# Kernel tuning notes

Hardware: AMD Instinct MI355X
Metric: run time of the kernel (lower is better)

The kernel has to match this reference:

```python
import jax, jax.numpy as jnp
import numpy as np

N_NODES = 100000
N_EDGES = 3200000
N_FEAT = 128
N_CLASS = 40
K_HOPS = 2


def setup_inputs() -> dict:
    key = jax.random.key(0)
    k1, k2, k3 = jax.random.split(key, 3)
    feature = jax.random.normal(k1, (N_NODES, N_FEAT), dtype=jnp.float32)
    # Glorot-ish linear params (SGConv.lin)
    weight = jax.random.normal(k2, (N_CLASS, N_FEAT), dtype=jnp.float32) * (1.0 / np.sqrt(N_FEAT))
    bias = jnp.zeros((N_CLASS,), dtype=jnp.float32)
    edge_index = jax.random.randint(k3, (2, N_EDGES), 0, N_NODES, dtype=jnp.int64)
    return {"feature": feature, "weight": weight, "bias": bias,
            "edge_index": edge_index, "use_feature": 1}


def reference(feature, weight, bias, edge_index, use_feature):
    # use_feature is a Python int flag; SGC uses feature when true (identity otherwise)
    x = feature if use_feature else jnp.eye(feature.shape[0], feature.shape[1], dtype=feature.dtype)
    N = x.shape[0]

    # gcn_norm: add self-loops, symmetric normalization D^-1/2 (A+I) D^-1/2
    loops = jnp.arange(N, dtype=edge_index.dtype)
    row = jnp.concatenate([edge_index[0], loops])  # source nodes
    col = jnp.concatenate([edge_index[1], loops])  # target nodes
    ew = jnp.ones(row.shape[0], dtype=x.dtype)
    deg = jax.ops.segment_sum(ew, col, num_segments=N)  # in-degree incl. self-loop
    deg_inv_sqrt = jnp.where(deg > 0, jax.lax.rsqrt(jnp.maximum(deg, 1e-12)), 0.0)
    norm = deg_inv_sqrt[row] * deg_inv_sqrt[col]  # [E+N]

    # K-hop propagation: out[col] += norm * x[row]
    for _ in range(K_HOPS):
        x = jax.ops.segment_sum(norm[:, None] * x[row], col, num_segments=N)

    logits = x @ weight.T + bias  # [N, C]
    return jax.nn.log_softmax(logits, axis=1)
```

## Files before the change

### kernel.cpp

```cpp
#include <hip/hip_runtime.h>
#include <hip/hip_bf16.h>
#include <hip/hip_fp16.h>
#include <math.h>


#define N_NODES 100000
#define N_FEAT  128
#define N_CLASS 40

#define RANGE   256
#define NBALLOC 512
#define NBUSED  391
#define CAP     8704
#define P3BLK   6250
#define HALF_SPLIT 50000

typedef __attribute__((ext_vector_type(8))) short short8;
typedef __attribute__((ext_vector_type(4))) float floatx4;

__device__ __forceinline__ int edge_word(const int* ei, int elem, int is64) {
    return is64 ? ei[2 * elem] : ei[elem];
}

__global__ __launch_bounds__(256) void p3a_scatter(
    const int* __restrict__ ei, int E,
    int* __restrict__ bucketCount, unsigned int* __restrict__ tmp)
{
    __shared__ unsigned int srt[P3BLK];
    __shared__ unsigned short fb[P3BLK];
    __shared__ int hist[NBALLOC];
    __shared__ int lbase[NBALLOC];
    __shared__ int gbase[NBALLOC];
    __shared__ int cur[NBALLOC];
    __shared__ int sc[256];
    __shared__ int s_is64;
    int t = threadIdx.x;
    for (int i = t; i < NBALLOC; i += 256) hist[i] = 0;
    if (t < 64) {
        int nz = (ei[2 * t + 1] != 0) ? 1 : 0;
        unsigned long long bl = __ballot(nz);
        if (t == 0) s_is64 = (bl == 0ull) ? 1 : 0;
    }
    __syncthreads();
    int is64 = s_is64;
    int per = (E + gridDim.x - 1) / gridDim.x;
    int e0 = blockIdx.x * per;
    int e1 = min(E, e0 + per);
    int n = e1 - e0;
    for (int e = e0 + t; e < e1; e += 256) {
        int c = edge_word(ei, E + e, is64);
        atomicAdd(&hist[c >> 8], 1);
    }
    __syncthreads();
    int h0 = hist[2 * t], h1 = hist[2 * t + 1];
    sc[t] = h0 + h1;
    __syncthreads();
    for (int o = 1; o < 256; o <<= 1) {
        int y = (t >= o) ? sc[t - o] : 0;
        __syncthreads();
        sc[t] += y;
        __syncthreads();
    }
    int excl = sc[t] - (h0 + h1);
    lbase[2 * t] = excl;
    lbase[2 * t + 1] = excl + h0;
    cur[2 * t] = excl;
    cur[2 * t + 1] = excl + h0;
    gbase[2 * t]     = h0 ? atomicAdd(&bucketCount[2 * t], h0) : 0;
    gbase[2 * t + 1] = h1 ? atomicAdd(&bucketCount[2 * t + 1], h1) : 0;
    __syncthreads();
    for (int e = e0 + t; e < e1; e += 256) {
        int c = edge_word(ei, E + e, is64);
        int r = edge_word(ei, e, is64);
        int f = c >> 8;
        int p = atomicAdd(&cur[f], 1);
        srt[p] = ((unsigned)(c & 255) << 24) | (unsigned)r;
        fb[p] = (unsigned short)f;
    }
    __syncthreads();
    for (int i = t; i < n; i += 256) {
        int f = fb[i];
        int p = gbase[f] + (i - lbase[f]);
        if (p < CAP) tmp[(size_t)f * CAP + p] = srt[i];
    }
}

__global__ __launch_bounds__(256) void p4_sort(
    const unsigned int* __restrict__ tmp, const int* __restrict__ bucketCount,
    int* __restrict__ starts, int* __restrict__ mid, float* __restrict__ dis,
    int* __restrict__ srcsB, int N, int E)
{
    __shared__ int srt[CAP];
    __shared__ int hist[512];
    __shared__ int sc[256];
    __shared__ int cur[512];
    __shared__ int cnt[NBALLOC];
    __shared__ int base_s;
    int b = blockIdx.x, t = threadIdx.x;
    int g0 = b * RANGE;
    int gcnt = N - g0;
    if (gcnt > RANGE) gcnt = RANGE;
    for (int i = t; i < NBALLOC; i += 256) cnt[i] = bucketCount[i];
    __syncthreads();
    int p0 = cnt[2 * t], p1 = cnt[2 * t + 1];
    sc[t] = p0 + p1;
    __syncthreads();
    for (int o = 1; o < 256; o <<= 1) {
        int y = (t >= o) ? sc[t - o] : 0;
        __syncthreads();
        sc[t] += y;
        __syncthreads();
    }
    if (t == 0) {
        int pairs = b >> 1;
        int base = (pairs > 0) ? sc[pairs - 1] : 0;
        if (b & 1) base += cnt[b - 1];
        base_s = base;
        if (b == 0) starts[N_NODES] = E;
    }
    __syncthreads();
    int base = base_s;
    int n = cnt[b];
    int nr = min(n, CAP);
    const unsigned int* rec = tmp + (size_t)b * CAP;
    hist[t] = 0;
    hist[t + 256] = 0;
    __syncthreads();
    for (int i = t; i < nr; i += 256) {
        unsigned v = rec[i];
        int key = (int)((v >> 24) << 1) | (((v & 0xFFFFFFu) >= HALF_SPLIT) ? 1 : 0);
        atomicAdd(&hist[key], 1);
    }
    __syncthreads();
    int c0 = hist[2 * t], c1 = hist[2 * t + 1];
    sc[t] = c0 + c1;
    __syncthreads();
    for (int o = 1; o < 256; o <<= 1) {
        int y = (t >= o) ? sc[t - o] : 0;
        __syncthreads();
        sc[t] += y;
        __syncthreads();
    }
    int excl = sc[t] - (c0 + c1);
    if (t < gcnt) {
        starts[g0 + t] = base + excl;
        mid[g0 + t] = base + excl + c0;
        dis[g0 + t] = rsqrtf((float)(c0 + c1 + 1));
    }
    cur[2 * t] = excl;
    cur[2 * t + 1] = excl + c0;
    __syncthreads();
    for (int i = t; i < nr; i += 256) {
        unsigned v = rec[i];
        int src = (int)(v & 0xFFFFFFu);
        int key = (int)((v >> 24) << 1) | ((src >= HALF_SPLIT) ? 1 : 0);
        int p = atomicAdd(&cur[key], 1);
        srt[p] = src * 80;
    }
    __syncthreads();
    for (int i = t; i < nr; i += 256) srcsB[base + i] = srt[i];
}

__device__ __forceinline__ unsigned short f2bf(float f) {
    unsigned u = __float_as_uint(f);
    unsigned r = u + 0x7FFFu + ((u >> 16) & 1u);
    return (unsigned short)(r >> 16);
}
__device__ __forceinline__ __half2 u2h(unsigned w) {
    union { unsigned u; __half2 h; } c; c.u = w; return c.h;
}
__device__ __forceinline__ unsigned h2u(__half2 h) {
    union { unsigned u; __half2 h; } c; c.h = h; return c.u;
}

__global__ __launch_bounds__(256) void transform_mfma(
    const float* __restrict__ x, const float* __restrict__ W,
    const float* __restrict__ dis, unsigned short* __restrict__ t0, int N)
{
    __shared__ uint4 Wl[3 * 4 * 64];
    int t = threadIdx.x;
    for (int i = t; i < 3 * 4 * 64; i += 256) {
        int lane = i & 63;
        int kc = (i >> 6) & 3;
        int nt = i >> 8;
        int n = nt * 16 + (lane & 15);
        int k = kc * 32 + (lane >> 4) * 8;
        union { unsigned short s[8]; uint4 v; } u;
        #pragma unroll
        for (int j = 0; j < 8; ++j)
            u.s[j] = (n < N_CLASS) ? f2bf(W[n * N_FEAT + k + j]) : (unsigned short)0;
        Wl[i] = u.v;
    }
    __syncthreads();
    int wave = (blockIdx.x * blockDim.x + threadIdx.x) >> 6;
    int lane = threadIdx.x & 63;
    int ntile = (N + 15) / 16;
    if (wave >= ntile) return;
    int m = lane & 15, quad = lane >> 4;
    int row = wave * 16 + m;
    const short8* Wf = reinterpret_cast<const short8*>(Wl);
    floatx4 acc0 = {0.f, 0.f, 0.f, 0.f}, acc1 = acc0, acc2 = acc0;
    #pragma unroll
    for (int kc = 0; kc < 4; ++kc) {
        const float4* xr = reinterpret_cast<const float4*>(
            x + (size_t)row * N_FEAT + kc * 32 + quad * 8);
        float4 a0 = xr[0], a1 = xr[1];
        short8 af;
        af[0] = f2bf(a0.x); af[1] = f2bf(a0.y); af[2] = f2bf(a0.z); af[3] = f2bf(a0.w);
        af[4] = f2bf(a1.x); af[5] = f2bf(a1.y); af[6] = f2bf(a1.z); af[7] = f2bf(a1.w);
        short8 b0 = Wf[(0 * 4 + kc) * 64 + lane];
        short8 b1 = Wf[(1 * 4 + kc) * 64 + lane];
        short8 b2 = Wf[(2 * 4 + kc) * 64 + lane];
        acc0 = __builtin_amdgcn_mfma_f32_16x16x32_bf16(af, b0, acc0, 0, 0, 0);
        acc1 = __builtin_amdgcn_mfma_f32_16x16x32_bf16(af, b1, acc1, 0, 0, 0);
        acc2 = __builtin_amdgcn_mfma_f32_16x16x32_bf16(af, b2, acc2, 0, 0, 0);
    }
    #pragma unroll
    for (int r = 0; r < 4; ++r) {
        int rw = wave * 16 + quad * 4 + r;
        float ds = dis[rw];
        unsigned short* tr = t0 + (size_t)rw * N_CLASS;
        tr[m] = __half_as_ushort(__float2half(ds * acc0[r]));
        tr[16 + m] = __half_as_ushort(__float2half(ds * acc1[r]));
        if (m < 8) tr[32 + m] = __half_as_ushort(__float2half(ds * acc2[r]));
    }
}

struct F8 { float v0, v1, v2, v3, v4, v5, v6, v7; };

__device__ __forceinline__ void acc8(F8& a, uint4 r) {
    float2 f0 = __half22float2(u2h(r.x));
    float2 f1 = __half22float2(u2h(r.y));
    float2 f2 = __half22float2(u2h(r.z));
    float2 f3 = __half22float2(u2h(r.w));
    a.v0 += f0.x; a.v1 += f0.y; a.v2 += f1.x; a.v3 += f1.y;
    a.v4 += f2.x; a.v5 += f2.y; a.v6 += f3.x; a.v7 += f3.y;
}

#define GATHERG(tin, eBp, eEp, SELFH)                                          \
    int wv = (blockIdx.x * blockDim.x + threadIdx.x) >> 6;                     \
    int lane = threadIdx.x & 63;                                               \
    int g = lane / 5;                                                          \
    int sl = lane - g * 5;                                                     \
    if (g > 11) { g = 11; sl = 0; }                                            \
    int d = wv * 12 + g;                                                       \
    int act = (lane < 60) && (d < N);                                          \
    int dc = min(d, N - 1);                                                    \
    int e0 = (eBp)[dc];                                                        \
    int e1 = (eEp)[dc];                                                        \
    if (d >= N) e1 = e0;                                                       \
    int slo = sl << 4;                                                         \
    const char* tbs = (const char*)(tin) + slo;                                \
    F8 A = {0,0,0,0,0,0,0,0}, B = {0,0,0,0,0,0,0,0};                           \
    if ((SELFH) ? (dc < HALF_SPLIT) : (dc >= HALF_SPLIT)) {                    \
        uint4 rs = *reinterpret_cast<const uint4*>(tbs + (size_t)dc * 80);     \
        acc8(A, rs);                                      \
    }                                                                          \
    int e = e0;                                                                \
    int ea = min(e1, (e0 + 3) & ~3);                                           \
    for (; e < ea; ++e) {                                   \
        unsigned o = (unsigned)srcsB[e];                                       \
        uint4 r = *reinterpret_cast<const uint4*>(tbs + o);                    \
        acc8(A, r);                                                            \
    }                                                                          \
    for (; e + 4 <= e1; e += 4) {                     \
        int4 o4 = *reinterpret_cast<const int4*>(srcsB + e);                   \
        uint4 r0 = *reinterpret_cast<const uint4*>(tbs + (unsigned)o4.x);      \
        uint4 r1 = *reinterpret_cast<const uint4*>(tbs + (unsigned)o4.y);      \
        uint4 r2 = *reinterpret_cast<const uint4*>(tbs + (unsigned)o4.z);      \
        uint4 r3 = *reinterpret_cast<const uint4*>(tbs + (unsigned)o4.w);      \
        acc8(A, r0); acc8(B, r1); acc8(A, r2); acc8(B, r3);                    \
    }                                                                          \
    for (; e < e1; ++e) {                                 \
        unsigned o = (unsigned)srcsB[e];                                       \
        uint4 r = *reinterpret_cast<const uint4*>(tbs + o);                    \
        acc8(A, r);                                                            \
    }                                                                          \
    A.v0 += B.v0; A.v1 += B.v1; A.v2 += B.v2; A.v3 += B.v3;                    \
    A.v4 += B.v4; A.v5 += B.v5; A.v6 += B.v6; A.v7 += B.v7;

__global__ __launch_bounds__(256) void prop_hop0(
    const unsigned short* __restrict__ tin, unsigned short* __restrict__ tout,
    const int* __restrict__ starts, const int* __restrict__ mid,
    const int* __restrict__ srcsB, int N)
{
    GATHERG(tin, starts, mid, 1)
    if (act) {
        uint4 o;
        o.x = h2u(__floats2half2_rn(A.v0, A.v1));
        o.y = h2u(__floats2half2_rn(A.v2, A.v3));
        o.z = h2u(__floats2half2_rn(A.v4, A.v5));
        o.w = h2u(__floats2half2_rn(A.v6, A.v7));
        *reinterpret_cast<uint4*>((char*)tout + (size_t)d * 80 + slo) = o;
    }
}

__global__ __launch_bounds__(256) void prop_hop1(
    const unsigned short* __restrict__ tin, unsigned short* __restrict__ tout,
    const int* __restrict__ starts, const int* __restrict__ mid,
    const int* __restrict__ srcsB, const float* __restrict__ dis, int N)
{
    GATHERG(tin, mid, starts + 1, 0)
    if (act) {
        uint4 pr = *reinterpret_cast<const uint4*>((const char*)tout + (size_t)d * 80 + slo);
        acc8(A, pr);
        float dd = dis[dc];
        float sc = dd * dd;
        uint4 o;
        o.x = h2u(__floats2half2_rn(sc * A.v0, sc * A.v1));
        o.y = h2u(__floats2half2_rn(sc * A.v2, sc * A.v3));
        o.z = h2u(__floats2half2_rn(sc * A.v4, sc * A.v5));
        o.w = h2u(__floats2half2_rn(sc * A.v6, sc * A.v7));
        *reinterpret_cast<uint4*>((char*)tout + (size_t)d * 80 + slo) = o;
    }
}

__global__ __launch_bounds__(256) void prop_fin0(
    const unsigned short* __restrict__ tin, float* __restrict__ out,
    const int* __restrict__ starts, const int* __restrict__ mid,
    const int* __restrict__ srcsB, int N)
{
    GATHERG(tin, starts, mid, 1)
    if (act) {
        float* ro = out + (size_t)d * N_CLASS + sl * 8;
        *reinterpret_cast<float4*>(ro)     = make_float4(A.v0, A.v1, A.v2, A.v3);
        *reinterpret_cast<float4*>(ro + 4) = make_float4(A.v4, A.v5, A.v6, A.v7);
    }
}

__global__ __launch_bounds__(256) void prop_fin1(
    const unsigned short* __restrict__ tin, float* __restrict__ out,
    const int* __restrict__ starts, const int* __restrict__ mid,
    const int* __restrict__ srcsB, const float* __restrict__ dis,
    const float* __restrict__ bias, int N)
{
    GATHERG(tin, mid, starts + 1, 0)
    float dd = dis[dc];
    const float* pp = out + (size_t)dc * N_CLASS + sl * 8;
    float4 plo = *reinterpret_cast<const float4*>(pp);
    float4 phi = *reinterpret_cast<const float4*>(pp + 4);
    float4 blo = reinterpret_cast<const float4*>(bias)[sl * 2];
    float4 bhi = reinterpret_cast<const float4*>(bias)[sl * 2 + 1];
    float v0 = dd * (plo.x + A.v0) + blo.x, v1 = dd * (plo.y + A.v1) + blo.y;
    float v2 = dd * (plo.z + A.v2) + blo.z, v3 = dd * (plo.w + A.v3) + blo.w;
    float v4 = dd * (phi.x + A.v4) + bhi.x, v5 = dd * (phi.y + A.v5) + bhi.y;
    float v6 = dd * (phi.z + A.v6) + bhi.z, v7 = dd * (phi.w + A.v7) + bhi.w;
    float mx = fmaxf(fmaxf(fmaxf(v0, v1), fmaxf(v2, v3)),
                     fmaxf(fmaxf(v4, v5), fmaxf(v6, v7)));
    int rot = g * 5 + ((sl + 1 == 5) ? 0 : sl + 1);
    float tmx = mx;
    #pragma unroll
    for (int k = 0; k < 4; ++k) { tmx = __shfl(tmx, rot); mx = fmaxf(mx, tmx); }
    float s = expf(v0 - mx) + expf(v1 - mx) + expf(v2 - mx) + expf(v3 - mx)
            + expf(v4 - mx) + expf(v5 - mx) + expf(v6 - mx) + expf(v7 - mx);
    float ts = s;
    #pragma unroll
    for (int k = 0; k < 4; ++k) { ts = __shfl(ts, rot); s += ts; }
    if (act) {
        float ls = mx + logf(s);
        float* ro = out + (size_t)d * N_CLASS + sl * 8;
        floatx4 lo = {v0 - ls, v1 - ls, v2 - ls, v3 - ls};
        floatx4 hi = {v4 - ls, v5 - ls, v6 - ls, v7 - ls};
        __builtin_nontemporal_store(lo, reinterpret_cast<floatx4*>(ro));
        __builtin_nontemporal_store(hi, reinterpret_cast<floatx4*>(ro) + 1);
    }
}

extern "C" void kernel_launch(void* const* d_in, const int* in_sizes, int n_in,
                              void* d_out, int out_size, void* d_ws, size_t ws_size,
                              hipStream_t stream) {
    const float* feature = (const float*)d_in[0];
    const float* weight  = (const float*)d_in[1];
    const float* bias    = (const float*)d_in[2];
    const int*   ei      = (const int*)d_in[3];
    const int N = N_NODES;
    const int E = in_sizes[3] / 2;

    size_t off = 0;
    auto take = [&](size_t bytes) { size_t o = off; off += (bytes + 255) & ~(size_t)255; return o; };
    char* ws = (char*)d_ws;
    int*   bCount    = (int*)  (ws + take((size_t)NBALLOC * 4));
    int*   starts    = (int*)  (ws + take((size_t)(N + 1) * 4));
    int*   mid       = (int*)  (ws + take((size_t)N * 4));
    float* dis       = (float*)(ws + take((size_t)N * 4));
    int*   srcsB     = (int*)  (ws + take((size_t)E * 4));
    unsigned short* t0 = (unsigned short*)(ws + take((size_t)N * N_CLASS * 2));
    unsigned short* t1 = (unsigned short*)(ws + take((size_t)N * N_CLASS * 2));
    unsigned int* tmp = (unsigned int*)t0;

    hipMemsetAsync(bCount, 0, (size_t)NBALLOC * 4, stream);
    const int p3grid = (E + P3BLK - 1) / P3BLK;
    p3a_scatter<<<p3grid, 256, 0, stream>>>(ei, E, bCount, tmp);
    p4_sort<<<NBUSED, 256, 0, stream>>>(tmp, bCount, starts, mid, dis, srcsB, N, E);

    const int ntile = (N + 15) / 16;
    const int tblocks = (ntile * 64 + 255) / 256;
    transform_mfma<<<tblocks, 256, 0, stream>>>(feature, weight, dis, t0, N);
    const int nwaves = (N + 11) / 12;
    const int nodeBlocks = (nwaves * 64 + 255) / 256;
    prop_hop0<<<nodeBlocks, 256, 0, stream>>>(t0, t1, starts, mid, srcsB, N);
    prop_hop1<<<nodeBlocks, 256, 0, stream>>>(t0, t1, starts, mid, srcsB, dis, N);
    prop_fin0<<<nodeBlocks, 256, 0, stream>>>(t1, (float*)d_out, starts, mid, srcsB, N);
    prop_fin1<<<nodeBlocks, 256, 0, stream>>>(t1, (float*)d_out, starts, mid, srcsB,
                                              dis, bias, N);
}
```

Measured before the change: 305.6 us.

## Merge split-half propagation kernels into single full-range gather per hop

Each hop previously ran as two kernels, each gathering one half of the edge list (split at mid). The second kernel re-read the partial result from global memory. Both halves are now gathered in one kernel, which removes two launches, the intermediate write and read-back of partial sums, and the extra index loads. The inner gather loop is also unrolled to 8 edges per iteration to raise memory-level parallelism. The trade-off is that the original split, presumably made for L2 locality on the source table halves, is lost, so each kernel now touches the whole table.

```diff
diff --git a/kernel.cpp b/kernel.cpp
--- a/kernel.cpp
+++ b/kernel.cpp
@@ -237,7 +237,47 @@
     a.v4 += f2.x; a.v5 += f2.y; a.v6 += f3.x; a.v7 += f3.y;
 }
 
-#define GATHERG(tin, eBp, eEp, SELFH)                                          \
+__device__ __forceinline__ void gather_range(
+    const char* tbs, const int* __restrict__ srcsB, int e0, int e1,
+    F8& A, F8& B)
+{
+    int e = e0;
+    int ea = min(e1, (e0 + 3) & ~3);
+    for (; e < ea; ++e) {
+        unsigned o = (unsigned)srcsB[e];
+        uint4 r = *reinterpret_cast<const uint4*>(tbs + o);
+        acc8(A, r);
+    }
+    for (; e + 8 <= e1; e += 8) {
+        int4 oa = *reinterpret_cast<const int4*>(srcsB + e);
+        int4 ob = *reinterpret_cast<const int4*>(srcsB + e + 4);
+        uint4 r0 = *reinterpret_cast<const uint4*>(tbs + (unsigned)oa.x);
+        uint4 r1 = *reinterpret_cast<const uint4*>(tbs + (unsigned)oa.y);
+        uint4 r2 = *reinterpret_cast<const uint4*>(tbs + (unsigned)oa.z);
+        uint4 r3 = *reinterpret_cast<const uint4*>(tbs + (unsigned)oa.w);
+        uint4 r4 = *reinterpret_cast<const uint4*>(tbs + (unsigned)ob.x);
+        uint4 r5 = *reinterpret_cast<const uint4*>(tbs + (unsigned)ob.y);
+        uint4 r6 = *reinterpret_cast<const uint4*>(tbs + (unsigned)ob.z);
+        uint4 r7 = *reinterpret_cast<const uint4*>(tbs + (unsigned)ob.w);
+        acc8(A, r0); acc8(B, r1); acc8(A, r2); acc8(B, r3);
+        acc8(A, r4); acc8(B, r5); acc8(A, r6); acc8(B, r7);
+    }
+    for (; e + 4 <= e1; e += 4) {
+        int4 o4 = *reinterpret_cast<const int4*>(srcsB + e);
+        uint4 r0 = *reinterpret_cast<const uint4*>(tbs + (unsigned)o4.x);
+        uint4 r1 = *reinterpret_cast<const uint4*>(tbs + (unsigned)o4.y);
+        uint4 r2 = *reinterpret_cast<const uint4*>(tbs + (unsigned)o4.z);
+        uint4 r3 = *reinterpret_cast<const uint4*>(tbs + (unsigned)o4.w);
+        acc8(A, r0); acc8(B, r1); acc8(A, r2); acc8(B, r3);
+    }
+    for (; e < e1; ++e) {
+        unsigned o = (unsigned)srcsB[e];
+        uint4 r = *reinterpret_cast<const uint4*>(tbs + o);
+        acc8(A, r);
+    }
+}
+
+#define GATHER_BOTH(tin)                                                       \
     int wv = (blockIdx.x * blockDim.x + threadIdx.x) >> 6;                     \
     int lane = threadIdx.x & 63;                                               \
     int g = lane / 5;                                                          \
@@ -246,64 +286,33 @@
     int d = wv * 12 + g;                                                       \
     int act = (lane < 60) && (d < N);                                          \
     int dc = min(d, N - 1);                                                    \
-    int e0 = (eBp)[dc];                                                        \
-    int e1 = (eEp)[dc];                                                        \
-    if (d >= N) e1 = e0;                                                       \
+    int e0 = starts[dc];                                                       \
+    int m  = mid[dc];                                                          \
+    int e1 = starts[dc + 1];                                                   \
+    if (d >= N) { m = e0; e1 = e0; }                                           \
     int slo = sl << 4;                                                         \
     const char* tbs = (const char*)(tin) + slo;                                \
     F8 A = {0,0,0,0,0,0,0,0}, B = {0,0,0,0,0,0,0,0};                           \
-    if ((SELFH) ? (dc < HALF_SPLIT) : (dc >= HALF_SPLIT)) {                    \
+    if (dc < HALF_SPLIT) {                            \
         uint4 rs = *reinterpret_cast<const uint4*>(tbs + (size_t)dc * 80);     \
-        acc8(A, rs);                                      \
+        acc8(A, rs);                                                           \
     }                                                                          \
-    int e = e0;                                                                \
-    int ea = min(e1, (e0 + 3) & ~3);                                           \
-    for (; e < ea; ++e) {                                   \
-        unsigned o = (unsigned)srcsB[e];                                       \
-        uint4 r = *reinterpret_cast<const uint4*>(tbs + o);                    \
-        acc8(A, r);                                                            \
+    gather_range(tbs, srcsB, e0, m, A, B);                    \
+    if (dc >= HALF_SPLIT) {                           \
+        uint4 rs = *reinterpret_cast<const uint4*>(tbs + (size_t)dc * 80);     \
+        acc8(A, rs);                                                           \
     }                                                                          \
-    for (; e + 4 <= e1; e += 4) {                     \
-        int4 o4 = *reinterpret_cast<const int4*>(srcsB + e);                   \
-        uint4 r0 = *reinterpret_cast<const uint4*>(tbs + (unsigned)o4.x);      \
-        uint4 r1 = *reinterpret_cast<const uint4*>(tbs + (unsigned)o4.y);      \
-        uint4 r2 = *reinterpret_cast<const uint4*>(tbs + (unsigned)o4.z);      \
-        uint4 r3 = *reinterpret_cast<const uint4*>(tbs + (unsigned)o4.w);      \
-        acc8(A, r0); acc8(B, r1); acc8(A, r2); acc8(B, r3);                    \
-    }                                                                          \
-    for (; e < e1; ++e) {                                 \
-        unsigned o = (unsigned)srcsB[e];                                       \
-        uint4 r = *reinterpret_cast<const uint4*>(tbs + o);                    \
-        acc8(A, r);                                                            \
-    }                                                                          \
+    gather_range(tbs, srcsB, m, e1, A, B);                    \
     A.v0 += B.v0; A.v1 += B.v1; A.v2 += B.v2; A.v3 += B.v3;                    \
     A.v4 += B.v4; A.v5 += B.v5; A.v6 += B.v6; A.v7 += B.v7;
 
-__global__ __launch_bounds__(256) void prop_hop0(
-    const unsigned short* __restrict__ tin, unsigned short* __restrict__ tout,
-    const int* __restrict__ starts, const int* __restrict__ mid,
-    const int* __restrict__ srcsB, int N)
-{
-    GATHERG(tin, starts, mid, 1)
-    if (act) {
-        uint4 o;
-        o.x = h2u(__floats2half2_rn(A.v0, A.v1));
-        o.y = h2u(__floats2half2_rn(A.v2, A.v3));
-        o.z = h2u(__floats2half2_rn(A.v4, A.v5));
-        o.w = h2u(__floats2half2_rn(A.v6, A.v7));
-        *reinterpret_cast<uint4*>((char*)tout + (size_t)d * 80 + slo) = o;
-    }
-}
-
-__global__ __launch_bounds__(256) void prop_hop1(
+__global__ __launch_bounds__(256) void prop_hop(
     const unsigned short* __restrict__ tin, unsigned short* __restrict__ tout,
     const int* __restrict__ starts, const int* __restrict__ mid,
     const int* __restrict__ srcsB, const float* __restrict__ dis, int N)
 {
-    GATHERG(tin, mid, starts + 1, 0)
+    GATHER_BOTH(tin)
     if (act) {
-        uint4 pr = *reinterpret_cast<const uint4*>((const char*)tout + (size_t)d * 80 + slo);
-        acc8(A, pr);
         float dd = dis[dc];
         float sc = dd * dd;
         uint4 o;
@@ -315,36 +324,20 @@
     }
 }
 
-__global__ __launch_bounds__(256) void prop_fin0(
-    const unsigned short* __restrict__ tin, float* __restrict__ out,
-    const int* __restrict__ starts, const int* __restrict__ mid,
-    const int* __restrict__ srcsB, int N)
-{
-    GATHERG(tin, starts, mid, 1)
-    if (act) {
-        float* ro = out + (size_t)d * N_CLASS + sl * 8;
-        *reinterpret_cast<float4*>(ro)     = make_float4(A.v0, A.v1, A.v2, A.v3);
-        *reinterpret_cast<float4*>(ro + 4) = make_float4(A.v4, A.v5, A.v6, A.v7);
-    }
-}
-
-__global__ __launch_bounds__(256) void prop_fin1(
+__global__ __launch_bounds__(256) void prop_fin(
     const unsigned short* __restrict__ tin, float* __restrict__ out,
     const int* __restrict__ starts, const int* __restrict__ mid,
     const int* __restrict__ srcsB, const float* __restrict__ dis,
     const float* __restrict__ bias, int N)
 {
-    GATHERG(tin, mid, starts + 1, 0)
+    GATHER_BOTH(tin)
     float dd = dis[dc];
-    const float* pp = out + (size_t)dc * N_CLASS + sl * 8;
-    float4 plo = *reinterpret_cast<const float4*>(pp);
-    float4 phi = *reinterpret_cast<const float4*>(pp + 4);
     float4 blo = reinterpret_cast<const float4*>(bias)[sl * 2];
     float4 bhi = reinterpret_cast<const float4*>(bias)[sl * 2 + 1];
-    float v0 = dd * (plo.x + A.v0) + blo.x, v1 = dd * (plo.y + A.v1) + blo.y;
-    float v2 = dd * (plo.z + A.v2) + blo.z, v3 = dd * (plo.w + A.v3) + blo.w;
-    float v4 = dd * (phi.x + A.v4) + bhi.x, v5 = dd * (phi.y + A.v5) + bhi.y;
-    float v6 = dd * (phi.z + A.v6) + bhi.z, v7 = dd * (phi.w + A.v7) + bhi.w;
+    float v0 = dd * A.v0 + blo.x, v1 = dd * A.v1 + blo.y;
+    float v2 = dd * A.v2 + blo.z, v3 = dd * A.v3 + blo.w;
+    float v4 = dd * A.v4 + bhi.x, v5 = dd * A.v5 + bhi.y;
+    float v6 = dd * A.v6 + bhi.z, v7 = dd * A.v7 + bhi.w;
     float mx = fmaxf(fmaxf(fmaxf(v0, v1), fmaxf(v2, v3)),
                      fmaxf(fmaxf(v4, v5), fmaxf(v6, v7)));
     int rot = g * 5 + ((sl + 1 == 5) ? 0 : sl + 1);
@@ -398,9 +391,7 @@
     transform_mfma<<<tblocks, 256, 0, stream>>>(feature, weight, dis, t0, N);
     const int nwaves = (N + 11) / 12;
     const int nodeBlocks = (nwaves * 64 + 255) / 256;
-    prop_hop0<<<nodeBlocks, 256, 0, stream>>>(t0, t1, starts, mid, srcsB, N);
-    prop_hop1<<<nodeBlocks, 256, 0, stream>>>(t0, t1, starts, mid, srcsB, dis, N);
-    prop_fin0<<<nodeBlocks, 256, 0, stream>>>(t1, (float*)d_out, starts, mid, srcsB, N);
-    prop_fin1<<<nodeBlocks, 256, 0, stream>>>(t1, (float*)d_out, starts, mid, srcsB,
-                                              dis, bias, N);
-}
+    prop_hop<<<nodeBlocks, 256, 0, stream>>>(t0, t1, starts, mid, srcsB, dis, N);
+    prop_fin<<<nodeBlocks, 256, 0, stream>>>(t1, (float*)d_out, starts, mid, srcsB,
+                                             dis, bias, N);
+}
```

Measured after the change: 283.3 us. 7.3% less time.
